# Kernel optimization log

Hardware: AMD Instinct MI355X
Metric: run time of the kernel (lower is better)

## Reference

```python
import jax, jax.numpy as jnp
import numpy as np

B, L, C = 2, 4096, 512
H, K = 8, 64
D = C // H
MIN_WINDOW = 1.0
SCALE_POWER = 0.3


def _rmsnorm(x, w, eps=1e-6):
    var = jnp.mean(x * x, axis=-1, keepdims=True)
    return w * (x * jax.lax.rsqrt(var + eps))


def setup_inputs() -> dict:
    key = jax.random.key(0)
    ks = jax.random.split(key, 16)
    n = jax.random.normal
    hid = max(C // 4, 8)
    return {
        "x": n(ks[0], (B, L, C), jnp.float32),
        "window_w": n(ks[1], (H, C), jnp.float32) * 0.02,
        "window_b": n(ks[2], (H,), jnp.float32) * 0.02,
        "window_gamma": jnp.ones((H,), jnp.float32),
        "offset_w": n(ks[3], (H, C), jnp.float32) * 0.02,
        "offset_b": n(ks[4], (H,), jnp.float32) * 0.02,
        "offset_gamma": jnp.ones((H,), jnp.float32),
        "kernel_w": n(ks[5], (H * K, C), jnp.float32) * 0.02,
        "kernel_b": n(ks[6], (H * K,), jnp.float32) * 0.02,
        "kernel_gamma": jnp.ones((H * K,), jnp.float32),
        "v_w": n(ks[7], (C, C), jnp.float32) * 0.02,
        "v_b": n(ks[8], (C,), jnp.float32) * 0.02,
        "se_w1": n(ks[9], (hid, C), jnp.float32) * 0.02,
        "se_w2": n(ks[10], (C, hid), jnp.float32) * 0.02,
        "out_w": n(ks[11], (C, C), jnp.float32) * 0.02,
    }


def reference(x, window_w, window_b, window_gamma, offset_w, offset_b, offset_gamma,
              kernel_w, kernel_b, kernel_gamma, v_w, v_b, se_w1, se_w2, out_w):
    dt = x.dtype
    max_window = min(int(L ** SCALE_POWER), K)          # 12 for L=4096
    half_max = max_window // 2                           # 6
    max_offset = float(int(L ** SCALE_POWER))            # 12
    S = 2 * half_max + 1                                 # 13 offsets

    # per-position learned window size, center offset, kernel weights
    window_raw = jax.nn.sigmoid(_rmsnorm(x @ window_w.T + window_b, window_gamma))
    window_sizes = MIN_WINDOW + window_raw * (max_window - MIN_WINDOW)   # (B,L,H)
    half_win = jnp.maximum(window_sizes * 0.5, 0.5)
    center_off = jnp.tanh(_rmsnorm(x @ offset_w.T + offset_b, offset_gamma)) * max_offset  # (B,L,H)
    kernel = jax.nn.silu(_rmsnorm(x @ kernel_w.T + kernel_b, kernel_gamma)).reshape(B, L, H, K)
    v = (x @ v_w.T + v_b).reshape(B, L, H, D)

    s_offs = jnp.arange(-half_max, half_max + 1, dtype=dt)               # (S,)
    pos = jnp.arange(L, dtype=dt)

    # gaussian window weight from relative distance  (B,L,H,S)
    rel = jnp.abs(s_offs) / half_win[..., None]
    win_w = jnp.exp(-rel * rel)

    # interpolate projected kernel weights along K by rel distance
    norm_pos = jnp.clip(rel, 0.0, 1.0) * (K - 1)
    idx_f = jnp.clip(norm_pos.astype(jnp.int32), 0, K - 2)
    w_c = norm_pos - idx_f.astype(dt)
    k_f = jnp.take_along_axis(kernel, idx_f, axis=-1)
    k_c = jnp.take_along_axis(kernel, idx_f + 1, axis=-1)
    ker_w = jnp.maximum(k_f * (1.0 - w_c) + k_c * w_c, 0.0)

    # deformable fractional neighbor positions  (B,L,H,S)
    nb = pos[None, :, None, None] + center_off[..., None] + s_offs
    valid = ((nb >= 0) & (nb < L)).astype(dt)
    weight = (ker_w + 1.0) * win_w * valid
    wsum = jnp.sum(weight, axis=-1)                                      # (B,L,H)

    pc = jnp.clip(nb, 0.0, L - 1.001)
    pf = jnp.clip(jnp.floor(pc).astype(jnp.int32), 0, L - 1)
    pcl = jnp.minimum(pf + 1, L - 1)
    frac = (pc - pf.astype(dt)).transpose(0, 2, 1, 3)                    # (B,H,L,S)

    vh = v.transpose(0, 2, 1, 3)                                         # (B,H,L,D)

    def gather(idx):  # idx (B,L,H,S) -> (B,H,L,S,D)
        it = idx.transpose(0, 2, 1, 3).reshape(B, H, L * S)
        return jnp.take_along_axis(vh, it[..., None], axis=2).reshape(B, H, L, S, D)

    val = gather(pf) * (1.0 - frac)[..., None] + gather(pcl) * frac[..., None]
    out_h = jnp.einsum('blhs,bhlsd->blhd', weight, val)
    out_h = out_h / jnp.maximum(wsum, 1.0)[..., None]
    out = out_h.reshape(B, L, C)

    # squeeze-excite over channels
    scale = jax.nn.sigmoid(jax.nn.silu(jnp.mean(out, axis=1) @ se_w1.T) @ se_w2.T)
    out = out * scale[:, None, :]
    return jax.nn.silu(out @ out_w.T)
```

## Files before the change

kernel.cpp:

```cpp
#include <hip/hip_runtime.h>
#include <hip/hip_bf16.h>
#include <cstddef>
#include <cstdint>


typedef _Float16 f16x8 __attribute__((ext_vector_type(8)));
typedef float f32x4 __attribute__((ext_vector_type(4)));

#define AS1 __attribute__((address_space(1)))
#define AS3 __attribute__((address_space(3)))

__device__ __forceinline__ void gload_lds16(const ushort* g, ushort* l) {
  __builtin_amdgcn_global_load_lds((const AS1 uint32_t*)g, (AS3 uint32_t*)l, 16, 0, 0);
}
__device__ __forceinline__ ushort f2h(float x) {
  _Float16 h = (_Float16)x;
  return __builtin_bit_cast(ushort, h);
}
__device__ __forceinline__ float h2f(ushort u) {
  return (float)__builtin_bit_cast(_Float16, u);
}
__device__ __forceinline__ float readlane_f(float v, int l) {
  return __int_as_float(__builtin_amdgcn_readlane(__float_as_int(v), l));
}

__global__ __launch_bounds__(256) void convert_h(
    const float* __restrict__ src, ushort* __restrict__ dst, int n4)
{
  for (int i = blockIdx.x * 256 + threadIdx.x; i < n4; i += gridDim.x * 256) {
    float4 v = ((const float4*)src)[i];
    ushort4 o = {f2h(v.x), f2h(v.y), f2h(v.z), f2h(v.w)};
    ((ushort4*)dst)[i] = o;
  }
}

__global__ __launch_bounds__(256) void scale_w_kernel(
    const float* __restrict__ out_w, const float* __restrict__ scalebuf,
    ushort* __restrict__ dst)
{
  const int i = blockIdx.x * 256 + threadIdx.x;
  const int b = i >> 16, iw = i & 65535, c4 = i & 127;
  float4 v = ((const float4*)out_w)[iw];
  float4 s = ((const float4*)scalebuf)[b * 128 + c4];
  ushort4 o = {f2h(v.x * s.x), f2h(v.y * s.y), f2h(v.z * s.z), f2h(v.w * s.w)};
  ((ushort4*)dst)[i] = o;
}

template<int MODE>
__global__ __launch_bounds__(256, 2) void gemm_mfma(
    const ushort* __restrict__ A, const ushort* __restrict__ B,
    const float* __restrict__ bk, const float* __restrict__ bv,
    ushort* __restrict__ Ck, ushort* __restrict__ Cv,
    float* __restrict__ Cf)
{
  __shared__ ushort smem[2 * 8192];
  const int t = threadIdx.x, wid = t >> 6, l = t & 63;

  const int bid = blockIdx.x;
  const int xcd = bid & 7, idx = bid >> 3;
  const int bx = (xcd << 3) | (idx & 7);
  const int by = idx >> 3;
  const int m0 = bx * 128, n0 = by * 128;

  const ushort* Bp = B;
  if (MODE == 1) Bp += (size_t)(m0 >> 12) << 18;

  const int swz = ((t & 7) ^ ((t >> 3) & 7)) * 8;
  const ushort* gsrc[8];
  uint32_t loff[8];
#pragma unroll
  for (int i = 0; i < 4; i++) {
    gsrc[i]     = A  + (size_t)(m0 + i * 32 + (t >> 3)) * 512 + swz;
    gsrc[4 + i] = Bp + (size_t)(n0 + i * 32 + (t >> 3)) * 512 + swz;
    loff[i]     = (i * 32 + wid * 8) * 64;
    loff[4 + i] = 8192 + (i * 32 + wid * 8) * 64;
  }

  f32x4 acc[4][4];
#pragma unroll
  for (int m = 0; m < 4; m++)
#pragma unroll
    for (int n = 0; n < 4; n++) acc[m][n] = (f32x4){0.f, 0.f, 0.f, 0.f};

  const int wr = wid >> 1, wc = wid & 1;
  const int fr = l & 15, fq = l >> 4;

  for (int k0 = 0; k0 < 512; k0 += 64) {
#pragma unroll
    for (int j = 0; j < 8; j++) {
      gload_lds16(gsrc[j], &smem[loff[j]]);
      gsrc[j] += 64;
    }
    __syncthreads();

    f16x8 af[4][2], bf[4][2];
#pragma unroll
    for (int m = 0; m < 4; m++)
#pragma unroll
      for (int ks = 0; ks < 2; ks++) {
        const int ko = 8 * ((ks * 4 + fq) ^ (fr & 7));
        af[m][ks] = *(const f16x8*)&smem[(wr * 64 + m * 16 + fr) * 64 + ko];
        bf[m][ks] = *(const f16x8*)&smem[8192 + (wc * 64 + m * 16 + fr) * 64 + ko];
      }
#pragma unroll
    for (int ks = 0; ks < 2; ks++)
#pragma unroll
      for (int m = 0; m < 4; m++)
#pragma unroll
        for (int n = 0; n < 4; n++)
          acc[m][n] = __builtin_amdgcn_mfma_f32_16x16x32_f16(af[m][ks], bf[n][ks], acc[m][n], 0, 0, 0);
    __syncthreads();
  }

  const int rbase = m0 + wr * 64 + (l >> 4) * 4;
  const int cbase = n0 + wc * 64 + (l & 15);
#pragma unroll
  for (int m = 0; m < 4; m++)
#pragma unroll
    for (int n = 0; n < 4; n++) {
      const int c = cbase + n * 16;
#pragma unroll
      for (int j = 0; j < 4; j++) {
        const int r = rbase + m * 16 + j;
        float v = acc[m][n][j];
        if (MODE == 0) {
          if (n0 < 512) Ck[(size_t)r * 512 + c]         = f2h(v + bk[c]);
          else          Cv[(size_t)r * 512 + (c - 512)] = f2h(v + bv[c - 512]);
        } else {
          Cf[(size_t)r * 512 + c] = v / (1.f + expf(-v));
        }
      }
    }
}

__global__ __launch_bounds__(256) void winoff_kernel(
    const float* __restrict__ x,
    const float* __restrict__ window_w, const float* __restrict__ window_b,
    const float* __restrict__ window_g,
    const float* __restrict__ offset_w, const float* __restrict__ offset_b,
    const float* __restrict__ offset_g,
    float* __restrict__ halfwin, float* __restrict__ cenoff,
    ushort* __restrict__ xh)
{
  __shared__ float wsm[16][512];
  const int t = threadIdx.x;
  {
    float4* dst = (float4*)&wsm[0][0];
    for (int i = t; i < 2048; i += 256)
      dst[i] = (i < 1024) ? ((const float4*)window_w)[i] : ((const float4*)offset_w)[i - 1024];
  }
  __syncthreads();
  const int wid = t >> 6, lane = t & 63;
  for (int it = 0; it < 4; it++) {
    const int row = blockIdx.x * 16 + it * 4 + wid;
    const float* xr = x + (size_t)row * 512;
    float xv[8];
#pragma unroll
    for (int j = 0; j < 8; j++) xv[j] = xr[lane + j * 64];
#pragma unroll
    for (int j = 0; j < 8; j++)
      xh[(size_t)row * 512 + lane + j * 64] = f2h(xv[j]);
    float s[16];
#pragma unroll
    for (int n = 0; n < 16; n++) {
      float p = 0.f;
#pragma unroll
      for (int j = 0; j < 8; j++) p += xv[j] * wsm[n][lane + j * 64];
#pragma unroll
      for (int off = 32; off >= 1; off >>= 1) p += __shfl_xor(p, off);
      s[n] = p;
    }
    float ssw = 0.f, sso = 0.f;
#pragma unroll
    for (int h = 0; h < 8; h++) {
      s[h]     += window_b[h]; ssw += s[h] * s[h];
      s[8 + h] += offset_b[h]; sso += s[8 + h] * s[8 + h];
    }
    float rw = rsqrtf(ssw * 0.125f + 1e-6f);
    float ro = rsqrtf(sso * 0.125f + 1e-6f);
    if (lane < 8) {
      float z  = window_g[lane] * s[lane] * rw;
      float wr2 = 1.f / (1.f + expf(-z));
      halfwin[(size_t)row * 8 + lane] = fmaxf((1.0f + wr2 * 11.0f) * 0.5f, 0.5f);
    } else if (lane < 16) {
      int h = lane - 8;
      float z = offset_g[h] * s[8 + h] * ro;
      cenoff[(size_t)row * 8 + h] = tanhf(z) * 12.0f;
    }
  }
}

__global__ __launch_bounds__(512) void conv_row_kernel(
    const float* __restrict__ halfwin, const float* __restrict__ cenoff,
    const ushort* __restrict__ kact_h, const float* __restrict__ kernel_g,
    const ushort* __restrict__ v_h, ushort* __restrict__ oh_h)
{
  __shared__ float kn[512];
  __shared__ float red[8];
  const int bid = blockIdx.x;
  const int row = ((bid & 7) << 10) | (bid >> 3);
  const int t = threadIdx.x, w = t >> 6, lane = t & 63;
  const int b = row >> 12, l = row & 4095;

  float kraw = h2f(kact_h[(size_t)row * 512 + t]);
  float ss = kraw * kraw;
#pragma unroll
  for (int off = 32; off >= 1; off >>= 1) ss += __shfl_xor(ss, off);
  if (lane == 0) red[w] = ss;
  __syncthreads();
  float tot = red[0] + red[1] + red[2] + red[3]
            + red[4] + red[5] + red[6] + red[7];
  float r = rsqrtf(tot * (1.f / 512.f) + 1e-6f);
  float a = kernel_g[t] * kraw * r;
  kn[t] = a / (1.f + __expf(-a));
  __syncthreads();

  const int gw = row * 8 + w;
  const float hw = halfwin[gw];
  const float co = cenoff[gw];
  const ushort* vbase = v_h + ((size_t)b * 4096) * 512 + w * 64 + lane;

  float wgt = 0.f, frv = 0.f;
  int pfv = 0;
  if (lane < 13) {
    const int soff = lane - 6;
    float rel  = fabsf((float)soff) / hw;
    float ww   = __expf(-rel * rel);
    float npos = fminf(rel, 1.f) * 63.f;
    int   idx  = min((int)npos, 62);
    float wc   = npos - (float)idx;
    float kf = kn[w * 64 + idx], kc = kn[w * 64 + idx + 1];
    float kw = fmaxf(kf * (1.f - wc) + kc * wc, 0.f);
    float nb = (float)l + co + (float)soff;
    wgt = (nb >= 0.f && nb < 4096.f) ? (kw + 1.f) * ww : 0.f;
    float pc = fminf(fmaxf(nb, 0.f), 4094.999f);
    pfv = (int)pc;
    frv = pc - (float)pfv;
  }
  float wsum = wgt;
#pragma unroll
  for (int off = 32; off >= 1; off >>= 1) wsum += __shfl_xor(wsum, off);

  const int base = __builtin_amdgcn_readlane(pfv, 0);
  const bool ok = (lane >= 13) || (pfv == base + lane);
  const bool fast = __all((int)ok) && (base + 13 <= 4095);

  float acc = 0.f;
  if (fast) {
    float wfr = wgt * frv;
    float w1f = wgt - wfr;
    float up  = __shfl_up(wfr, 1);
    float u = (lane < 13 ? w1f : 0.f) + ((lane >= 1 && lane <= 13) ? up : 0.f);
    const ushort* vr = vbase + (size_t)base * 512;
    float xv[14];
#pragma unroll
    for (int rr = 0; rr < 14; rr++) xv[rr] = h2f(vr[(size_t)rr * 512]);
#pragma unroll
    for (int rr = 0; rr < 14; rr++) acc = fmaf(readlane_f(u, rr), xv[rr], acc);
  } else {
#pragma unroll
    for (int si = 0; si < 13; si++) {
      const float w_s  = readlane_f(wgt, si);
      const float fr_s = readlane_f(frv, si);
      const int   pf_s = __builtin_amdgcn_readlane(pfv, si);
      const int   pcl  = min(pf_s + 1, 4095);
      float v0 = h2f(vbase[(size_t)pf_s * 512]);
      float v1 = h2f(vbase[(size_t)pcl * 512]);
      float t0 = v0 + fr_s * (v1 - v0);
      acc = fmaf(w_s, t0, acc);
    }
  }

  float val = acc / fmaxf(wsum, 1.f);
  oh_h[(size_t)row * 512 + w * 64 + lane] = f2h(val);
}

__global__ __launch_bounds__(256) void colpart_kernel(
    const ushort* __restrict__ oh_h, float* __restrict__ partial)
{
  const int blk = blockIdx.x;
  const int b = blk >> 6, chunk = blk & 63;
  const int t = threadIdx.x;
  const size_t base = ((size_t)b * 4096 + (size_t)chunk * 64) * 512;
  float s0 = 0.f, s1 = 0.f;
  for (int i = 0; i < 64; i++) {
    uint u = *(const uint*)(oh_h + base + (size_t)i * 512 + t * 2);
    s0 += h2f((ushort)(u & 0xffffu));
    s1 += h2f((ushort)(u >> 16));
  }
  partial[(size_t)blk * 512 + t * 2]     = s0;
  partial[(size_t)blk * 512 + t * 2 + 1] = s1;
}

__global__ __launch_bounds__(256) void se_hid_kernel(
    const float* __restrict__ partial, const float* __restrict__ w1,
    float* __restrict__ hid_g)
{
  const int wid = threadIdx.x >> 6, lane = threadIdx.x & 63;
  const int g = blockIdx.x * 4 + wid;
  const int b2 = g >> 7, j = g & 127;
  float4 m0 = {0.f, 0.f, 0.f, 0.f}, m1 = {0.f, 0.f, 0.f, 0.f};
#pragma unroll 8
  for (int ch = 0; ch < 64; ch++) {
    const float4* pr = (const float4*)(partial + (size_t)(b2 * 64 + ch) * 512);
    float4 a0 = pr[lane * 2], a1 = pr[lane * 2 + 1];
    m0.x += a0.x; m0.y += a0.y; m0.z += a0.z; m0.w += a0.w;
    m1.x += a1.x; m1.y += a1.y; m1.z += a1.z; m1.w += a1.w;
  }
  float4 wv0 = ((const float4*)(w1 + (size_t)j * 512))[lane * 2];
  float4 wv1 = ((const float4*)(w1 + (size_t)j * 512))[lane * 2 + 1];
  float p = (wv0.x * m0.x + wv0.y * m0.y + wv0.z * m0.z + wv0.w * m0.w
           + wv1.x * m1.x + wv1.y * m1.y + wv1.z * m1.z + wv1.w * m1.w) * (1.f / 4096.f);
#pragma unroll
  for (int off = 32; off >= 1; off >>= 1) p += __shfl_xor(p, off);
  if (lane == 0) hid_g[g] = p / (1.f + expf(-p));
}

__global__ __launch_bounds__(256) void se_scale_kernel(
    const float* __restrict__ hid_g, const float* __restrict__ w2,
    float* __restrict__ scalebuf)
{
  const int wid = threadIdx.x >> 6, lane = threadIdx.x & 63;
  const int g = blockIdx.x * 4 + wid;
  const int b3 = g >> 9, c = g & 511;
  float2 wv = ((const float2*)(w2 + (size_t)c * 128))[lane];
  float2 hv = ((const float2*)(hid_g + b3 * 128))[lane];
  float p = wv.x * hv.x + wv.y * hv.y;
#pragma unroll
  for (int off = 32; off >= 1; off >>= 1) p += __shfl_xor(p, off);
  if (lane == 0) scalebuf[g] = 1.f / (1.f + expf(-p));
}

extern "C" void kernel_launch(void* const* d_in, const int* in_sizes, int n_in,
                              void* d_out, int out_size, void* d_ws, size_t ws_size,
                              hipStream_t stream) {
  const float* x        = (const float*)d_in[0];
  const float* window_w = (const float*)d_in[1];
  const float* window_b = (const float*)d_in[2];
  const float* window_g = (const float*)d_in[3];
  const float* offset_w = (const float*)d_in[4];
  const float* offset_b = (const float*)d_in[5];
  const float* offset_g = (const float*)d_in[6];
  const float* kernel_w = (const float*)d_in[7];
  const float* kernel_b = (const float*)d_in[8];
  const float* kernel_g = (const float*)d_in[9];
  const float* v_w      = (const float*)d_in[10];
  const float* v_b      = (const float*)d_in[11];
  const float* se_w1    = (const float*)d_in[12];
  const float* se_w2    = (const float*)d_in[13];
  const float* out_w    = (const float*)d_in[14];
  float* out = (float*)d_out;
  char* ws   = (char*)d_ws;

  const size_t BLC = (size_t)8192 * 512;
  float* halfwin  = (float*)ws;                       ws += 65536 * 4;
  float* cenoff   = (float*)ws;                       ws += 65536 * 4;
  float* partial  = (float*)ws;                       ws += 128 * 512 * 4;
  float* hid_g    = (float*)ws;                       ws += 256 * 4;
  float* scalebuf = (float*)ws;                       ws += 1024 * 4;
  ushort* xh      = (ushort*)ws;                      ws += BLC * 2;
  ushort* wkv_h   = (ushort*)ws;                      ws += 1024 * 512 * 2;
  ushort* kact_h  = (ushort*)ws;                      ws += BLC * 2;
  ushort* v_h     = (ushort*)ws;                      ws += BLC * 2;
  ushort* oh_h    = (ushort*)ws;                      ws += BLC * 2;
  ushort* ow_h    = (ushort*)ws;                      ws += 2 * 512 * 512 * 2;

  winoff_kernel<<<512, 256, 0, stream>>>(x, window_w, window_b, window_g,
                                         offset_w, offset_b, offset_g,
                                         halfwin, cenoff, xh);
  convert_h<<<256, 256, 0, stream>>>(kernel_w, wkv_h, 65536);
  convert_h<<<256, 256, 0, stream>>>(v_w, wkv_h + 262144, 65536);

  gemm_mfma<0><<<512, 256, 0, stream>>>(xh, wkv_h, kernel_b, v_b,
                                        kact_h, v_h, nullptr);
  conv_row_kernel<<<8192, 512, 0, stream>>>(halfwin, cenoff, kact_h, kernel_g,
                                            v_h, oh_h);
  colpart_kernel<<<128, 256, 0, stream>>>(oh_h, partial);
  se_hid_kernel<<<64, 256, 0, stream>>>(partial, se_w1, hid_g);
  se_scale_kernel<<<256, 256, 0, stream>>>(hid_g, se_w2, scalebuf);
  scale_w_kernel<<<512, 256, 0, stream>>>(out_w, scalebuf, ow_h);
  gemm_mfma<1><<<256, 256, 0, stream>>>(oh_h, ow_h, nullptr, nullptr,
                                        nullptr, nullptr, out);
}
```

Measured before the change: 91.23 us.

## Fuse weight conversion into winoff and SE chain into one cooperative kernel

Folds the fp16 conversion of the kernel and v weights into extra blocks of winoff_kernel, and merges the four SE-stage kernels into one cooperative kernel with grid-wide syncs. Replaces the LDS kernel-weight table in conv_row with wave shuffles, vectorizes the x loads, and splits the accumulator into two chains. Also swaps expf/tanhf for fast __expf-based forms. The goal is fewer launches and less synchronisation, at the cost of cooperative-launch overhead and small accuracy changes.

```diff
diff --git a/kernel.cpp b/kernel.cpp
--- a/kernel.cpp
+++ b/kernel.cpp
@@ -1,7 +1,10 @@
 #include <hip/hip_runtime.h>
 #include <hip/hip_bf16.h>
+#include <hip/hip_cooperative_groups.h>
 #include <cstddef>
 #include <cstdint>
+
+namespace cg = cooperative_groups;
 
 
 typedef _Float16 f16x8 __attribute__((ext_vector_type(8)));
@@ -23,28 +26,7 @@
 __device__ __forceinline__ float readlane_f(float v, int l) {
   return __int_as_float(__builtin_amdgcn_readlane(__float_as_int(v), l));
 }
-
-__global__ __launch_bounds__(256) void convert_h(
-    const float* __restrict__ src, ushort* __restrict__ dst, int n4)
-{
-  for (int i = blockIdx.x * 256 + threadIdx.x; i < n4; i += gridDim.x * 256) {
-    float4 v = ((const float4*)src)[i];
-    ushort4 o = {f2h(v.x), f2h(v.y), f2h(v.z), f2h(v.w)};
-    ((ushort4*)dst)[i] = o;
-  }
-}
-
-__global__ __launch_bounds__(256) void scale_w_kernel(
-    const float* __restrict__ out_w, const float* __restrict__ scalebuf,
-    ushort* __restrict__ dst)
-{
-  const int i = blockIdx.x * 256 + threadIdx.x;
-  const int b = i >> 16, iw = i & 65535, c4 = i & 127;
-  float4 v = ((const float4*)out_w)[iw];
-  float4 s = ((const float4*)scalebuf)[b * 128 + c4];
-  ushort4 o = {f2h(v.x * s.x), f2h(v.y * s.y), f2h(v.z * s.z), f2h(v.w * s.w)};
-  ((ushort4*)dst)[i] = o;
-}
+__device__ __forceinline__ float sigm(float z) { return 1.f / (1.f + __expf(-z)); }
 
 template<int MODE>
 __global__ __launch_bounds__(256, 2) void gemm_mfma(
@@ -127,7 +109,7 @@
           if (n0 < 512) Ck[(size_t)r * 512 + c]         = f2h(v + bk[c]);
           else          Cv[(size_t)r * 512 + (c - 512)] = f2h(v + bv[c - 512]);
         } else {
-          Cf[(size_t)r * 512 + c] = v / (1.f + expf(-v));
+          Cf[(size_t)r * 512 + c] = v * sigm(v);
         }
       }
     }
@@ -140,10 +122,21 @@
     const float* __restrict__ offset_w, const float* __restrict__ offset_b,
     const float* __restrict__ offset_g,
     float* __restrict__ halfwin, float* __restrict__ cenoff,
-    ushort* __restrict__ xh)
+    ushort* __restrict__ xh,
+    const float* __restrict__ kernel_w, const float* __restrict__ v_w,
+    ushort* __restrict__ wkv_h)
 {
+  const int t = threadIdx.x;
+  if (blockIdx.x >= 512) {
+    for (int i = (blockIdx.x - 512) * 256 + t; i < 131072; i += 32768) {
+      float4 v = (i < 65536) ? ((const float4*)kernel_w)[i]
+                             : ((const float4*)v_w)[i - 65536];
+      ushort4 o = {f2h(v.x), f2h(v.y), f2h(v.z), f2h(v.w)};
+      ((ushort4*)wkv_h)[i] = o;
+    }
+    return;
+  }
   __shared__ float wsm[16][512];
-  const int t = threadIdx.x;
   {
     float4* dst = (float4*)&wsm[0][0];
     for (int i = t; i < 2048; i += 256)
@@ -153,19 +146,19 @@
   const int wid = t >> 6, lane = t & 63;
   for (int it = 0; it < 4; it++) {
     const int row = blockIdx.x * 16 + it * 4 + wid;
-    const float* xr = x + (size_t)row * 512;
-    float xv[8];
-#pragma unroll
-    for (int j = 0; j < 8; j++) xv[j] = xr[lane + j * 64];
-#pragma unroll
-    for (int j = 0; j < 8; j++)
-      xh[(size_t)row * 512 + lane + j * 64] = f2h(xv[j]);
+    const float4* xr4 = (const float4*)(x + (size_t)row * 512);
+    float4 a0 = xr4[lane * 2], a1 = xr4[lane * 2 + 1];
+    ushort4 h0 = {f2h(a0.x), f2h(a0.y), f2h(a0.z), f2h(a0.w)};
+    ushort4 h1 = {f2h(a1.x), f2h(a1.y), f2h(a1.z), f2h(a1.w)};
+    ((ushort4*)(xh + (size_t)row * 512))[lane * 2]     = h0;
+    ((ushort4*)(xh + (size_t)row * 512))[lane * 2 + 1] = h1;
     float s[16];
 #pragma unroll
     for (int n = 0; n < 16; n++) {
-      float p = 0.f;
-#pragma unroll
-      for (int j = 0; j < 8; j++) p += xv[j] * wsm[n][lane + j * 64];
+      const float4* wr = (const float4*)&wsm[n][0];
+      float4 w0 = wr[lane * 2], w1 = wr[lane * 2 + 1];
+      float p = a0.x * w0.x + a0.y * w0.y + a0.z * w0.z + a0.w * w0.w
+              + a1.x * w1.x + a1.y * w1.y + a1.z * w1.z + a1.w * w1.w;
 #pragma unroll
       for (int off = 32; off >= 1; off >>= 1) p += __shfl_xor(p, off);
       s[n] = p;
@@ -179,13 +172,13 @@
     float rw = rsqrtf(ssw * 0.125f + 1e-6f);
     float ro = rsqrtf(sso * 0.125f + 1e-6f);
     if (lane < 8) {
-      float z  = window_g[lane] * s[lane] * rw;
-      float wr2 = 1.f / (1.f + expf(-z));
-      halfwin[(size_t)row * 8 + lane] = fmaxf((1.0f + wr2 * 11.0f) * 0.5f, 0.5f);
+      float z = window_g[lane] * s[lane] * rw;
+      halfwin[(size_t)row * 8 + lane] = fmaxf((1.0f + sigm(z) * 11.0f) * 0.5f, 0.5f);
     } else if (lane < 16) {
       int h = lane - 8;
       float z = offset_g[h] * s[8 + h] * ro;
-      cenoff[(size_t)row * 8 + h] = tanhf(z) * 12.0f;
+      float th = 1.f - 2.f / (__expf(2.f * z) + 1.f);
+      cenoff[(size_t)row * 8 + h] = th * 12.0f;
     }
   }
 }
@@ -195,7 +188,6 @@
     const ushort* __restrict__ kact_h, const float* __restrict__ kernel_g,
     const ushort* __restrict__ v_h, ushort* __restrict__ oh_h)
 {
-  __shared__ float kn[512];
   __shared__ float red[8];
   const int bid = blockIdx.x;
   const int row = ((bid & 7) << 10) | (bid >> 3);
@@ -212,31 +204,28 @@
             + red[4] + red[5] + red[6] + red[7];
   float r = rsqrtf(tot * (1.f / 512.f) + 1e-6f);
   float a = kernel_g[t] * kraw * r;
-  kn[t] = a / (1.f + __expf(-a));
-  __syncthreads();
+  float kn_l = a * sigm(a);
 
   const int gw = row * 8 + w;
   const float hw = halfwin[gw];
   const float co = cenoff[gw];
   const ushort* vbase = v_h + ((size_t)b * 4096) * 512 + w * 64 + lane;
 
-  float wgt = 0.f, frv = 0.f;
-  int pfv = 0;
-  if (lane < 13) {
-    const int soff = lane - 6;
-    float rel  = fabsf((float)soff) / hw;
-    float ww   = __expf(-rel * rel);
-    float npos = fminf(rel, 1.f) * 63.f;
-    int   idx  = min((int)npos, 62);
-    float wc   = npos - (float)idx;
-    float kf = kn[w * 64 + idx], kc = kn[w * 64 + idx + 1];
-    float kw = fmaxf(kf * (1.f - wc) + kc * wc, 0.f);
-    float nb = (float)l + co + (float)soff;
-    wgt = (nb >= 0.f && nb < 4096.f) ? (kw + 1.f) * ww : 0.f;
-    float pc = fminf(fmaxf(nb, 0.f), 4094.999f);
-    pfv = (int)pc;
-    frv = pc - (float)pfv;
-  }
+  const float soff = (float)(lane - 6);
+  float rel  = fabsf(soff) / hw;
+  float ww   = __expf(-rel * rel);
+  float npos = fminf(rel, 1.f) * 63.f;
+  int   idxk = min((int)npos, 62);
+  float wc   = npos - (float)idxk;
+  float kf = __shfl(kn_l, idxk);
+  float kc = __shfl(kn_l, idxk + 1);
+  float kw = fmaxf(kf * (1.f - wc) + kc * wc, 0.f);
+  float nb = (float)l + co + soff;
+  float wgt = (lane < 13 && nb >= 0.f && nb < 4096.f) ? (kw + 1.f) * ww : 0.f;
+  float pc  = fminf(fmaxf(nb, 0.f), 4094.999f);
+  int   pfv = (int)pc;
+  float frv = pc - (float)pfv;
+
   float wsum = wgt;
 #pragma unroll
   for (int off = 32; off >= 1; off >>= 1) wsum += __shfl_xor(wsum, off);
@@ -245,7 +234,7 @@
   const bool ok = (lane >= 13) || (pfv == base + lane);
   const bool fast = __all((int)ok) && (base + 13 <= 4095);
 
-  float acc = 0.f;
+  float acc0 = 0.f, acc1 = 0.f;
   if (fast) {
     float wfr = wgt * frv;
     float w1f = wgt - wfr;
@@ -256,7 +245,10 @@
 #pragma unroll
     for (int rr = 0; rr < 14; rr++) xv[rr] = h2f(vr[(size_t)rr * 512]);
 #pragma unroll
-    for (int rr = 0; rr < 14; rr++) acc = fmaf(readlane_f(u, rr), xv[rr], acc);
+    for (int rr = 0; rr < 14; rr += 2) {
+      acc0 = fmaf(readlane_f(u, rr),     xv[rr],     acc0);
+      acc1 = fmaf(readlane_f(u, rr + 1), xv[rr + 1], acc1);
+    }
   } else {
 #pragma unroll
     for (int si = 0; si < 13; si++) {
@@ -266,69 +258,80 @@
       const int   pcl  = min(pf_s + 1, 4095);
       float v0 = h2f(vbase[(size_t)pf_s * 512]);
       float v1 = h2f(vbase[(size_t)pcl * 512]);
-      float t0 = v0 + fr_s * (v1 - v0);
-      acc = fmaf(w_s, t0, acc);
-    }
-  }
-
-  float val = acc / fmaxf(wsum, 1.f);
+      acc0 = fmaf(w_s, v0 + fr_s * (v1 - v0), acc0);
+    }
+  }
+
+  float val = (acc0 + acc1) / fmaxf(wsum, 1.f);
   oh_h[(size_t)row * 512 + w * 64 + lane] = f2h(val);
 }
 
-__global__ __launch_bounds__(256) void colpart_kernel(
-    const ushort* __restrict__ oh_h, float* __restrict__ partial)
+__global__ __launch_bounds__(256) void se_coop_kernel(
+    const ushort* __restrict__ oh_h,
+    const float* __restrict__ w1, const float* __restrict__ w2,
+    const float* __restrict__ out_w,
+    float* __restrict__ partial, float* __restrict__ hid_g,
+    float* __restrict__ scalebuf, ushort* __restrict__ ow_h)
 {
-  const int blk = blockIdx.x;
-  const int b = blk >> 6, chunk = blk & 63;
-  const int t = threadIdx.x;
-  const size_t base = ((size_t)b * 4096 + (size_t)chunk * 64) * 512;
-  float s0 = 0.f, s1 = 0.f;
-  for (int i = 0; i < 64; i++) {
-    uint u = *(const uint*)(oh_h + base + (size_t)i * 512 + t * 2);
-    s0 += h2f((ushort)(u & 0xffffu));
-    s1 += h2f((ushort)(u >> 16));
-  }
-  partial[(size_t)blk * 512 + t * 2]     = s0;
-  partial[(size_t)blk * 512 + t * 2 + 1] = s1;
-}
-
-__global__ __launch_bounds__(256) void se_hid_kernel(
-    const float* __restrict__ partial, const float* __restrict__ w1,
-    float* __restrict__ hid_g)
-{
-  const int wid = threadIdx.x >> 6, lane = threadIdx.x & 63;
-  const int g = blockIdx.x * 4 + wid;
-  const int b2 = g >> 7, j = g & 127;
-  float4 m0 = {0.f, 0.f, 0.f, 0.f}, m1 = {0.f, 0.f, 0.f, 0.f};
+  cg::grid_group grid = cg::this_grid();
+  const int blk = blockIdx.x, t = threadIdx.x;
+  const int wid = t >> 6, lane = t & 63;
+
+  {
+    const int b = blk >> 6, chunk = blk & 63;
+    const size_t base = ((size_t)b * 4096 + (size_t)chunk * 64) * 512;
+    float s0 = 0.f, s1 = 0.f;
+    for (int i = 0; i < 64; i++) {
+      uint u = *(const uint*)(oh_h + base + (size_t)i * 512 + t * 2);
+      s0 += h2f((ushort)(u & 0xffffu));
+      s1 += h2f((ushort)(u >> 16));
+    }
+    partial[(size_t)blk * 512 + t * 2]     = s0;
+    partial[(size_t)blk * 512 + t * 2 + 1] = s1;
+  }
+  grid.sync();
+
+  if (blk < 64) {
+    const int g = blk * 4 + wid;
+    const int b2 = g >> 7, j = g & 127;
+    float4 m0 = {0.f, 0.f, 0.f, 0.f}, m1 = {0.f, 0.f, 0.f, 0.f};
 #pragma unroll 8
-  for (int ch = 0; ch < 64; ch++) {
-    const float4* pr = (const float4*)(partial + (size_t)(b2 * 64 + ch) * 512);
-    float4 a0 = pr[lane * 2], a1 = pr[lane * 2 + 1];
-    m0.x += a0.x; m0.y += a0.y; m0.z += a0.z; m0.w += a0.w;
-    m1.x += a1.x; m1.y += a1.y; m1.z += a1.z; m1.w += a1.w;
-  }
-  float4 wv0 = ((const float4*)(w1 + (size_t)j * 512))[lane * 2];
-  float4 wv1 = ((const float4*)(w1 + (size_t)j * 512))[lane * 2 + 1];
-  float p = (wv0.x * m0.x + wv0.y * m0.y + wv0.z * m0.z + wv0.w * m0.w
-           + wv1.x * m1.x + wv1.y * m1.y + wv1.z * m1.z + wv1.w * m1.w) * (1.f / 4096.f);
-#pragma unroll
-  for (int off = 32; off >= 1; off >>= 1) p += __shfl_xor(p, off);
-  if (lane == 0) hid_g[g] = p / (1.f + expf(-p));
-}
-
-__global__ __launch_bounds__(256) void se_scale_kernel(
-    const float* __restrict__ hid_g, const float* __restrict__ w2,
-    float* __restrict__ scalebuf)
-{
-  const int wid = threadIdx.x >> 6, lane = threadIdx.x & 63;
-  const int g = blockIdx.x * 4 + wid;
-  const int b3 = g >> 9, c = g & 511;
-  float2 wv = ((const float2*)(w2 + (size_t)c * 128))[lane];
-  float2 hv = ((const float2*)(hid_g + b3 * 128))[lane];
-  float p = wv.x * hv.x + wv.y * hv.y;
-#pragma unroll
-  for (int off = 32; off >= 1; off >>= 1) p += __shfl_xor(p, off);
-  if (lane == 0) scalebuf[g] = 1.f / (1.f + expf(-p));
+    for (int ch = 0; ch < 64; ch++) {
+      const float4* pr = (const float4*)(partial + (size_t)(b2 * 64 + ch) * 512);
+      float4 a0 = pr[lane * 2], a1 = pr[lane * 2 + 1];
+      m0.x += a0.x; m0.y += a0.y; m0.z += a0.z; m0.w += a0.w;
+      m1.x += a1.x; m1.y += a1.y; m1.z += a1.z; m1.w += a1.w;
+    }
+    float4 wv0 = ((const float4*)(w1 + (size_t)j * 512))[lane * 2];
+    float4 wv1 = ((const float4*)(w1 + (size_t)j * 512))[lane * 2 + 1];
+    float p = (wv0.x * m0.x + wv0.y * m0.y + wv0.z * m0.z + wv0.w * m0.w
+             + wv1.x * m1.x + wv1.y * m1.y + wv1.z * m1.z + wv1.w * m1.w) * (1.f / 4096.f);
+#pragma unroll
+    for (int off = 32; off >= 1; off >>= 1) p += __shfl_xor(p, off);
+    if (lane == 0) hid_g[g] = p * sigm(p);
+  }
+  grid.sync();
+
+#pragma unroll
+  for (int rep = 0; rep < 2; rep++) {
+    const int g = (blk * 4 + wid) * 2 + rep;
+    const int b3 = g >> 9, c = g & 511;
+    float2 wv = ((const float2*)(w2 + (size_t)c * 128))[lane];
+    float2 hv = ((const float2*)(hid_g + b3 * 128))[lane];
+    float p = wv.x * hv.x + wv.y * hv.y;
+#pragma unroll
+    for (int off = 32; off >= 1; off >>= 1) p += __shfl_xor(p, off);
+    if (lane == 0) scalebuf[g] = sigm(p);
+  }
+  grid.sync();
+
+  for (int i = blk * 256 + t; i < 131072; i += 32768) {
+    const int b = i >> 16, iw = i & 65535, c4 = i & 127;
+    float4 v = ((const float4*)out_w)[iw];
+    float4 s = ((const float4*)scalebuf)[b * 128 + c4];
+    ushort4 o = {f2h(v.x * s.x), f2h(v.y * s.y), f2h(v.z * s.z), f2h(v.w * s.w)};
+    ((ushort4*)ow_h)[i] = o;
+  }
 }
 
 extern "C" void kernel_launch(void* const* d_in, const int* in_sizes, int n_in,
@@ -365,20 +368,20 @@
   ushort* oh_h    = (ushort*)ws;                      ws += BLC * 2;
   ushort* ow_h    = (ushort*)ws;                      ws += 2 * 512 * 512 * 2;
 
-  winoff_kernel<<<512, 256, 0, stream>>>(x, window_w, window_b, window_g,
+  winoff_kernel<<<640, 256, 0, stream>>>(x, window_w, window_b, window_g,
                                          offset_w, offset_b, offset_g,
-                                         halfwin, cenoff, xh);
-  convert_h<<<256, 256, 0, stream>>>(kernel_w, wkv_h, 65536);
-  convert_h<<<256, 256, 0, stream>>>(v_w, wkv_h + 262144, 65536);
-
+                                         halfwin, cenoff, xh,
+                                         kernel_w, v_w, wkv_h);
   gemm_mfma<0><<<512, 256, 0, stream>>>(xh, wkv_h, kernel_b, v_b,
                                         kact_h, v_h, nullptr);
   conv_row_kernel<<<8192, 512, 0, stream>>>(halfwin, cenoff, kact_h, kernel_g,
                                             v_h, oh_h);
-  colpart_kernel<<<128, 256, 0, stream>>>(oh_h, partial);
-  se_hid_kernel<<<64, 256, 0, stream>>>(partial, se_w1, hid_g);
-  se_scale_kernel<<<256, 256, 0, stream>>>(hid_g, se_w2, scalebuf);
-  scale_w_kernel<<<512, 256, 0, stream>>>(out_w, scalebuf, ow_h);
+  {
+    void* args[] = {(void*)&oh_h, (void*)&se_w1, (void*)&se_w2, (void*)&out_w,
+                    (void*)&partial, (void*)&hid_g, (void*)&scalebuf, (void*)&ow_h};
+    hipLaunchCooperativeKernel((const void*)se_coop_kernel, dim3(128), dim3(256),
+                               args, 0, stream);
+  }
   gemm_mfma<1><<<256, 256, 0, stream>>>(oh_h, ow_h, nullptr, nullptr,
                                         nullptr, nullptr, out);
 }
```

New measurement: 137.6 us. 50.8% more time.
